# Kernel tuning notes

Hardware: AMD Instinct MI355X
Metric: run time of the kernel (lower is better)

The kernel has to match this reference:

```python
import jax, jax.numpy as jnp
import numpy as np

N = 100000       # num nodes
E = 1000000      # num edges
D_IN = 128       # input feature dim
D_H = 64         # hidden = output dim
EPS = 1e-5       # GraphNorm eps
SLOPE = 0.2      # LeakyReLU negative slope


def _glorot(key, shape):
    lim = float(np.sqrt(6.0 / (shape[0] + shape[1])))
    return jax.random.uniform(key, shape, jnp.float32, -lim, lim)


def setup_inputs() -> dict:
    key = jax.random.key(0)
    ks = jax.random.split(key, 6)
    return {
        "x": jax.random.normal(ks[0], (N, D_IN), jnp.float32),
        "edge_index": jax.random.randint(ks[1], (2, E), 0, N),
        "W_in": _glorot(ks[2], (D_IN, D_H)),
        "b_in": jnp.zeros((D_H,), jnp.float32),
        "W1": _glorot(ks[3], (D_H, D_H)),
        "b1": jnp.zeros((D_H,), jnp.float32),
        "gn1_alpha": jnp.ones((D_H,), jnp.float32),
        "gn1_gamma": jnp.ones((D_H,), jnp.float32),
        "gn1_beta": jnp.zeros((D_H,), jnp.float32),
        "W2": _glorot(ks[4], (D_H, D_H)),
        "b2": jnp.zeros((D_H,), jnp.float32),
        "gn2_alpha": jnp.ones((D_H,), jnp.float32),
        "gn2_gamma": jnp.ones((D_H,), jnp.float32),
        "gn2_beta": jnp.zeros((D_H,), jnp.float32),
    }


def gcn_conv(x, W, b, src, dst):
    # GCNConv with added self-loops and symmetric normalization:
    # out = D^{-1/2} (A + I) D^{-1/2} (x W) + b
    xw = x @ W                                                 # [N, D]
    ones = jnp.ones((src.shape[0],), x.dtype)
    deg = jax.ops.segment_sum(ones, dst, num_segments=x.shape[0]) + 1.0  # +1 self-loop
    dinv = jax.lax.rsqrt(deg)                                  # [N]
    coef = dinv[src] * dinv[dst]                               # [E]
    agg = jax.ops.segment_sum(xw[src] * coef[:, None], dst, num_segments=x.shape[0])
    return agg + xw * (dinv * dinv)[:, None] + b


def graph_norm(x, alpha, gamma, beta):
    # PyG GraphNorm over a single graph: per-feature mean/var over all nodes
    mean = jnp.mean(x, axis=0)
    c = x - alpha * mean
    var = jnp.mean(c * c, axis=0)
    return gamma * c * jax.lax.rsqrt(var + EPS) + beta


def reference(x, edge_index, W_in, b_in, W1, b1, gn1_alpha, gn1_gamma, gn1_beta,
              W2, b2, gn2_alpha, gn2_gamma, gn2_beta):
    src, dst = edge_index[0], edge_index[1]
    h = x @ W_in + b_in                                        # input projection
    h = graph_norm(gcn_conv(h, W1, b1, src, dst), gn1_alpha, gn1_gamma, gn1_beta)
    h = jnp.where(h > 0, h, SLOPE * h)                         # LeakyReLU(0.2); dropout=eval (identity)
    h = graph_norm(gcn_conv(h, W2, b2, src, dst), gn2_alpha, gn2_gamma, gn2_beta)
    return h                                                    # [N, D_H]
```

## Files before the change

kernel.cpp:

```cpp
#include <hip/hip_runtime.h>
#include <stdint.h>

#define N_NODES 100000
#define N_EDGES 1000000
#define D_IN 128
#define D_H 64
#define EPS 1e-5f
#define SLOPE 0.2f

typedef unsigned short u16;
typedef unsigned int u32;
typedef __attribute__((ext_vector_type(8))) short bf16x8;
typedef __attribute__((ext_vector_type(4))) float f32x4;

__device__ __forceinline__ float bf2f(u16 u) {
    union { u32 i; float f; } v; v.i = ((u32)u) << 16; return v.f;
}
__device__ __forceinline__ u16 f2bf(float f) {
    union { float f; u32 i; } v; v.f = f;
    u32 r = (v.i + 0x7fffu + ((v.i >> 16) & 1u)) >> 16;
    return (u16)r;
}
__device__ __forceinline__ bool is_f32(const void* flagp) {
    return *(const u32*)flagp == 0x3F800000u;
}
__device__ __forceinline__ float loadf(const void* p, size_t i, bool m) {
    return m ? ((const float*)p)[i] : bf2f(((const u16*)p)[i]);
}

__global__ void kprep(const void* __restrict__ W_in, const void* __restrict__ b_in,
                      const void* __restrict__ W1, const void* __restrict__ W2,
                      const void* __restrict__ flagp,
                      u16* __restrict__ WcT, u16* __restrict__ W2T,
                      float* __restrict__ bc, u16* __restrict__ xwb_pad)
{
    bool m = is_f32(flagp);
    int t = threadIdx.x;
    if (blockIdx.x < 64) {
        int c = blockIdx.x;
        __shared__ float w1c[D_H];
        if (t < D_H) w1c[t] = loadf(W1, t * D_H + c, m);
        __syncthreads();
        float acc = 0.f;
        #pragma unroll 8
        for (int j = 0; j < D_H; j++) acc += loadf(W_in, t * D_H + j, m) * w1c[j];
        WcT[c * D_IN + t] = f2bf(acc);
        if (t == 0) {
            float b = 0.f;
            for (int j = 0; j < D_H; j++) b += loadf(b_in, j, m) * w1c[j];
            bc[c] = b;
        }
        if (c == 0 && t < D_H) xwb_pad[(size_t)N_NODES * D_H + t] = 0;
    } else {
        int idx = (blockIdx.x - 64) * 128 + t;
        int n = idx >> 6, k = idx & 63;
        W2T[n * D_H + k] = f2bf(loadf(W2, k * D_H + n, m));
    }
}

__global__ void kfill(const int* __restrict__ ei, int* __restrict__ cnt,
                      int* __restrict__ bucket)
{
    int e = blockIdx.x * blockDim.x + threadIdx.x;
    if (e >= N_EDGES) return;
    int s = ei[e];
    int d = ei[N_EDGES + e];
    int slot = atomicAdd(&cnt[d], 1);
    if (slot < 64) bucket[(size_t)d * 64 + slot] = s;
}

__global__ __launch_bounds__(256) void kgemm1(const void* __restrict__ x,
        const u16* __restrict__ WcT, const float* __restrict__ bc,
        const int* __restrict__ cnt, const void* __restrict__ flagp,
        u16* __restrict__ xwb)
{
    bool m = is_f32(flagp);
    __shared__ __align__(16) u16 xs[64 * 136];
    __shared__ __align__(16) u16 WT[64 * 136];
    int tid = threadIdx.x;
    int row0 = blockIdx.x * 64;
    for (int i = tid; i < 64 * 32; i += 256) {
        int r = i >> 5, kq = (i & 31) * 4;
        *(ushort4*)(WT + r * 136 + kq) = *(const ushort4*)(WcT + r * D_IN + kq);
    }
    for (int i = tid; i < 64 * 32; i += 256) {
        int r = i >> 5, kq = (i & 31) * 4;
        int gr = row0 + r;
        ushort4 u = make_ushort4(0, 0, 0, 0);
        if (gr < N_NODES) {
            if (m) {
                float4 v = *(const float4*)((const float*)x + (size_t)gr * D_IN + kq);
                u = make_ushort4(f2bf(v.x), f2bf(v.y), f2bf(v.z), f2bf(v.w));
            } else {
                u = *(const ushort4*)((const u16*)x + (size_t)gr * D_IN + kq);
            }
        }
        *(ushort4*)(xs + r * 136 + kq) = u;
    }
    __syncthreads();
    int w = tid >> 6, L = tid & 63;
    int q = L >> 4, c = L & 15;
    f32x4 acc[4];
    #pragma unroll
    for (int ct = 0; ct < 4; ct++) {
        float b = bc[ct * 16 + c];
        acc[ct] = (f32x4){b, b, b, b};
    }
    const u16* ap = xs + (w * 16 + c) * 136 + q * 8;
    #pragma unroll
    for (int kk = 0; kk < 4; kk++) {
        bf16x8 af = *(const bf16x8*)(ap + kk * 32);
        #pragma unroll
        for (int ct = 0; ct < 4; ct++) {
            bf16x8 bfr = *(const bf16x8*)(WT + (ct * 16 + c) * 136 + kk * 32 + q * 8);
            acc[ct] = __builtin_amdgcn_mfma_f32_16x16x32_bf16(af, bfr, acc[ct], 0, 0, 0);
        }
    }
    #pragma unroll
    for (int r = 0; r < 4; r++) {
        int gr = row0 + w * 16 + q * 4 + r;
        if (gr < N_NODES) {
            float ds = rsqrtf((float)cnt[gr] + 1.0f);
            #pragma unroll
            for (int ct = 0; ct < 4; ct++)
                xwb[(size_t)gr * D_H + ct * 16 + c] = f2bf(acc[ct][r] * ds);
        }
    }
}

__global__ __launch_bounds__(256) void kagg(const u16* __restrict__ xwb,
        const int* __restrict__ cnt, const int* __restrict__ bucket,
        const void* __restrict__ bvec, const void* __restrict__ flagp,
        u16* __restrict__ ybuf, float* __restrict__ accum)
{
    bool m = is_f32(flagp);
    __shared__ __align__(16) char smem[4][8192];
    __shared__ float red_s[4][64], red_q[4][64];
    int tid = threadIdx.x;
    int wv = tid >> 6, L = tid & 63;
    int half = L >> 5, mm = L & 31;
    int node0 = blockIdx.x * 32 + wv * 8;

    int cnt8 = cnt[node0 + (L & 7)];
    int deg[8]; float dd[8];
    #pragma unroll
    for (int t = 0; t < 8; t++) {
        int cv = __builtin_amdgcn_readlane(cnt8, t);
        deg[t] = min(cv, 64);
        dd[t] = rsqrtf((float)cv + 1.0f);
    }
    float b0 = loadf(bvec, 2 * mm, m), b1 = loadf(bvec, 2 * mm + 1, m);

    int tl = L >> 4, sl = L & 15;
    int raw0 = bucket[(size_t)(node0 + tl) * 64 + sl];
    int raw1 = bucket[(size_t)(node0 + 4 + tl) * 64 + sl];

    float ls0 = 0, ls1 = 0, lq0 = 0, lq1 = 0;
    char* base = &smem[wv][0];

    #pragma unroll
    for (int b = 0; b < 2; b++) {
        int nb = node0 + b * 4;
        int raw = b ? raw1 : raw0;
        int i_l = nb + tl;
        int degL = min(__shfl(cnt8, b * 4 + tl), 64);
        int src = (sl < degL) ? raw : ((sl == degL) ? i_l : N_NODES);

        #pragma unroll
        for (int k = 0; k < 8; k++) {
            if ((k & 1) == 0 || deg[b * 4 + (k >> 1)] + 1 > 8) {
                int srcK = __shfl(src, k * 8 + (L >> 3));
                const u16* gp = xwb + (size_t)srcK * D_H + (L & 7) * 8;
                __builtin_amdgcn_global_load_lds(gp, base + k * 1024, 16, 0, 0);
            }
        }
        __builtin_amdgcn_s_waitcnt(0);
        __builtin_amdgcn_sched_barrier(0);
        asm volatile("" ::: "memory");

        float A0 = 0, A1 = 0, C0 = 0, C1 = 0;
        #pragma unroll
        for (int p = 0; p < 2; p++) {
            int np = p * 2 + half;
            const u32* rp = (const u32*)(base + np * 2048);
            int dnp = half ? deg[b * 4 + p * 2 + 1] : deg[b * 4 + p * 2];
            float a0 = 0, a1 = 0;
            #pragma unroll
            for (int s = 0; s < 8; s++) {
                u32 v = rp[s * 32 + mm];
                a0 += __uint_as_float(v << 16);
                a1 += __uint_as_float(v & 0xffff0000u);
            }
            if (dnp + 1 > 8) {
                #pragma unroll
                for (int s = 8; s < 16; s++) {
                    u32 v = rp[s * 32 + mm];
                    a0 += __uint_as_float(v << 16);
                    a1 += __uint_as_float(v & 0xffff0000u);
                }
            }
            if (p == 0) { A0 = a0; A1 = a1; } else { C0 = a0; C1 = a1; }
        }
        #pragma unroll
        for (int t = 0; t < 4; t++) {
            int degt = deg[b * 4 + t];
            if (degt >= 16) {
                int i = nb + t;
                float r0 = 0, r1 = 0;
                for (int s = 16 + half; s <= degt; s += 2) {
                    int sv = (s < degt) ? bucket[(size_t)i * 64 + s] : i;
                    u32 v = *((const u32*)(xwb + (size_t)sv * D_H) + mm);
                    r0 += __uint_as_float(v << 16);
                    r1 += __uint_as_float(v & 0xffff0000u);
                }
                r0 += __shfl_xor(r0, 32);
                r1 += __shfl_xor(r1, 32);
                bool mine = (half == (t & 1));
                if (t < 2) { A0 += mine ? r0 : 0.f; A1 += mine ? r1 : 0.f; }
                else       { C0 += mine ? r0 : 0.f; C1 += mine ? r1 : 0.f; }
            }
        }
        #pragma unroll
        for (int p = 0; p < 2; p++) {
            float a0 = p ? C0 : A0, a1 = p ? C1 : A1;
            float ddv = half ? dd[b * 4 + p * 2 + 1] : dd[b * 4 + p * 2];
            float y0 = ddv * a0 + b0;
            float y1 = ddv * a1 + b1;
            int node = nb + p * 2 + half;
            ((u32*)(ybuf + (size_t)node * D_H))[mm] =
                (u32)f2bf(y0) | ((u32)f2bf(y1) << 16);
            ls0 += y0; ls1 += y1; lq0 += y0 * y0; lq1 += y1 * y1;
        }
        asm volatile("" ::: "memory");
    }

    ls0 += __shfl_xor(ls0, 32); ls1 += __shfl_xor(ls1, 32);
    lq0 += __shfl_xor(lq0, 32); lq1 += __shfl_xor(lq1, 32);
    if (half == 0) {
        *(float2*)&red_s[wv][2 * mm] = make_float2(ls0, ls1);
        *(float2*)&red_q[wv][2 * mm] = make_float2(lq0, lq1);
    }
    __syncthreads();
    if (tid < 64) {
        atomicAdd(&accum[tid],      red_s[0][tid] + red_s[1][tid] + red_s[2][tid] + red_s[3][tid]);
        atomicAdd(&accum[64 + tid], red_q[0][tid] + red_q[1][tid] + red_q[2][tid] + red_q[3][tid]);
    }
}

__global__ __launch_bounds__(256) void kgemm2(const u16* __restrict__ y1b,
        const u16* __restrict__ W2T, const float* __restrict__ accum,
        const void* __restrict__ alpha, const void* __restrict__ gamma,
        const void* __restrict__ beta, const void* __restrict__ flagp,
        const int* __restrict__ cnt, u16* __restrict__ xwb)
{
    bool m = is_f32(flagp);
    __shared__ __align__(16) u16 hs[64 * 72];
    __shared__ __align__(16) u16 WT[64 * 72];
    __shared__ float aL[64], cL[64];
    int tid = threadIdx.x;
    if (tid < 64) {
        float mean = accum[tid] * (1.0f / N_NODES);
        float al = loadf(alpha, tid, m);
        float var = accum[64 + tid] * (1.0f / N_NODES) - mean * mean * al * (2.0f - al);
        var = fmaxf(var, 0.f);
        float a = loadf(gamma, tid, m) * rsqrtf(var + EPS);
        aL[tid] = a;
        cL[tid] = loadf(beta, tid, m) - a * al * mean;
    }
    for (int i = tid; i < 64 * 16; i += 256) {
        int r = i >> 4, kq = (i & 15) * 4;
        *(ushort4*)(WT + r * 72 + kq) = *(const ushort4*)(W2T + r * D_H + kq);
    }
    __syncthreads();
    int row0 = blockIdx.x * 64;
    for (int i = tid; i < 64 * 16; i += 256) {
        int r = i >> 4, kq = (i & 15) * 4;
        int gr = row0 + r;
        ushort4 u = make_ushort4(0, 0, 0, 0);
        if (gr < N_NODES) u = *(const ushort4*)(y1b + (size_t)gr * D_H + kq);
        float h0 = aL[kq + 0] * bf2f(u.x) + cL[kq + 0]; h0 = h0 > 0.f ? h0 : SLOPE * h0;
        float h1 = aL[kq + 1] * bf2f(u.y) + cL[kq + 1]; h1 = h1 > 0.f ? h1 : SLOPE * h1;
        float h2 = aL[kq + 2] * bf2f(u.z) + cL[kq + 2]; h2 = h2 > 0.f ? h2 : SLOPE * h2;
        float h3 = aL[kq + 3] * bf2f(u.w) + cL[kq + 3]; h3 = h3 > 0.f ? h3 : SLOPE * h3;
        *(ushort4*)(hs + r * 72 + kq) = make_ushort4(f2bf(h0), f2bf(h1), f2bf(h2), f2bf(h3));
    }
    __syncthreads();
    int w = tid >> 6, L = tid & 63;
    int q = L >> 4, c = L & 15;
    f32x4 acc[4] = {};
    const u16* ap = hs + (w * 16 + c) * 72 + q * 8;
    #pragma unroll
    for (int kk = 0; kk < 2; kk++) {
        bf16x8 af = *(const bf16x8*)(ap + kk * 32);
        #pragma unroll
        for (int ct = 0; ct < 4; ct++) {
            bf16x8 bfr = *(const bf16x8*)(WT + (ct * 16 + c) * 72 + kk * 32 + q * 8);
            acc[ct] = __builtin_amdgcn_mfma_f32_16x16x32_bf16(af, bfr, acc[ct], 0, 0, 0);
        }
    }
    #pragma unroll
    for (int r = 0; r < 4; r++) {
        int gr = row0 + w * 16 + q * 4 + r;
        if (gr < N_NODES) {
            float ds = rsqrtf((float)cnt[gr] + 1.0f);
            #pragma unroll
            for (int ct = 0; ct < 4; ct++)
                xwb[(size_t)gr * D_H + ct * 16 + c] = f2bf(acc[ct][r] * ds);
        }
    }
}

__global__ __launch_bounds__(256) void kout(const u16* __restrict__ y2b,
        const float* __restrict__ accum2, const void* __restrict__ alpha,
        const void* __restrict__ gamma, const void* __restrict__ beta,
        const void* __restrict__ flagp, void* __restrict__ out)
{
    bool m = is_f32(flagp);
    __shared__ float a2[64], c2[64];
    int tid = threadIdx.x;
    if (tid < 64) {
        float mean = accum2[tid] * (1.0f / N_NODES);
        float al = loadf(alpha, tid, m);
        float var = accum2[64 + tid] * (1.0f / N_NODES) - mean * mean * al * (2.0f - al);
        var = fmaxf(var, 0.f);
        float a = loadf(gamma, tid, m) * rsqrtf(var + EPS);
        a2[tid] = a;
        c2[tid] = loadf(beta, tid, m) - a * al * mean;
    }
    __syncthreads();
    int w0 = (blockIdx.x * 256 + tid) * 2;
    u32 v0 = ((const u32*)y2b)[w0];
    u32 v1 = ((const u32*)y2b)[w0 + 1];
    int f = (w0 * 2) & 63;
    float o0 = a2[f + 0] * __uint_as_float(v0 << 16)          + c2[f + 0];
    float o1 = a2[f + 1] * __uint_as_float(v0 & 0xffff0000u)  + c2[f + 1];
    float o2 = a2[f + 2] * __uint_as_float(v1 << 16)          + c2[f + 2];
    float o3 = a2[f + 3] * __uint_as_float(v1 & 0xffff0000u)  + c2[f + 3];
    if (m) {
        *(float4*)((float*)out + (size_t)w0 * 2) = make_float4(o0, o1, o2, o3);
    } else {
        u32 p0 = (u32)f2bf(o0) | ((u32)f2bf(o1) << 16);
        u32 p1 = (u32)f2bf(o2) | ((u32)f2bf(o3) << 16);
        *(uint2*)((u32*)out + w0) = make_uint2(p0, p1);
    }
}

extern "C" void kernel_launch(void* const* d_in, const int* in_sizes, int n_in,
                              void* d_out, int out_size, void* d_ws, size_t ws_size,
                              hipStream_t stream)
{
    const void* x    = d_in[0];
    const int*  ei   = (const int*)d_in[1];
    const void* W_in = d_in[2];
    const void* b_in = d_in[3];
    const void* W1   = d_in[4];
    const void* b1   = d_in[5];
    const void* gn1a = d_in[6];
    const void* gn1g = d_in[7];
    const void* gn1b = d_in[8];
    const void* W2   = d_in[9];
    const void* b2   = d_in[10];
    const void* gn2a = d_in[11];
    const void* gn2g = d_in[12];
    const void* gn2b = d_in[13];

    char* ws = (char*)d_ws;
    int*   cnt    = (int*)(ws + 0);
    float* accum  = (float*)(ws + 400000);
    float* bc     = (float*)(ws + 402048);
    u16*   WcT    = (u16*)(ws + 402432);
    u16*   W2T    = (u16*)(ws + 418816);
    int*   bucket = (int*)(ws + 1235200);
    u16*   bufA   = (u16*)(ws + 26835200);
    u16*   bufB   = (u16*)(ws + 39635456);

    hipMemsetAsync(ws, 0, 400000 + 1024, stream);

    kprep<<<96, 128, 0, stream>>>(W_in, b_in, W1, W2, gn1a, WcT, W2T, bc, bufA);
    kfill<<<(N_EDGES + 255) / 256, 256, 0, stream>>>(ei, cnt, bucket);
    kgemm1<<<(N_NODES + 63) / 64, 256, 0, stream>>>(x, WcT, bc, cnt, gn1a, bufA);
    kagg<<<N_NODES / 32, 256, 0, stream>>>(bufA, cnt, bucket, b1, gn1a, bufB, accum);
    kgemm2<<<(N_NODES + 63) / 64, 256, 0, stream>>>(bufB, W2T, accum, gn1a, gn1g, gn1b, gn1a, cnt, bufA);
    kagg<<<N_NODES / 32, 256, 0, stream>>>(bufA, cnt, bucket, b2, gn1a, bufB, accum + 128);
    kout<<<N_NODES * D_H / 1024, 256, 0, stream>>>(bufB, accum + 128, gn2a, gn2g, gn2b, gn1a, d_out);
}
```

Baseline: 397.2 us.

## Replace LDS-staged neighbor gather with register double-buffered direct loads in aggregation

The aggregation kernel no longer stages neighbor rows into shared memory with global_load_lds and a full waitcnt barrier. Each half-wave now gathers its node's 16 neighbor slots straight into registers and prefetches the next node's 16 rows while summing the current ones, so loads overlap with compute across four node groups. This removes the LDS round trip and the per-batch stalls, but always issues 16 loads per node, including padded slots that point at the dummy row, and roughly doubles the register footprint for the gather buffers.

```diff
diff --git a/kernel.cpp b/kernel.cpp
--- a/kernel.cpp
+++ b/kernel.cpp
@@ -134,7 +134,6 @@
         u16* __restrict__ ybuf, float* __restrict__ accum)
 {
     bool m = is_f32(flagp);
-    __shared__ __align__(16) char smem[4][8192];
     __shared__ float red_s[4][64], red_q[4][64];
     int tid = threadIdx.x;
     int wv = tid >> 6, L = tid & 63;
@@ -142,96 +141,64 @@
     int node0 = blockIdx.x * 32 + wv * 8;
 
     int cnt8 = cnt[node0 + (L & 7)];
-    int deg[8]; float dd[8];
-    #pragma unroll
-    for (int t = 0; t < 8; t++) {
-        int cv = __builtin_amdgcn_readlane(cnt8, t);
-        deg[t] = min(cv, 64);
-        dd[t] = rsqrtf((float)cv + 1.0f);
-    }
-    float b0 = loadf(bvec, 2 * mm, m), b1 = loadf(bvec, 2 * mm + 1, m);
-
     int tl = L >> 4, sl = L & 15;
     int raw0 = bucket[(size_t)(node0 + tl) * 64 + sl];
     int raw1 = bucket[(size_t)(node0 + 4 + tl) * 64 + sl];
 
+    float b0 = loadf(bvec, 2 * mm, m), b1 = loadf(bvec, 2 * mm + 1, m);
     float ls0 = 0, ls1 = 0, lq0 = 0, lq1 = 0;
-    char* base = &smem[wv][0];
-
-    #pragma unroll
-    for (int b = 0; b < 2; b++) {
-        int nb = node0 + b * 4;
-        int raw = b ? raw1 : raw0;
-        int i_l = nb + tl;
-        int degL = min(__shfl(cnt8, b * 4 + tl), 64);
-        int src = (sl < degL) ? raw : ((sl == degL) ? i_l : N_NODES);
-
+
+    const char* xb = (const char*)xwb;
+    u32 moff = (u32)(mm << 2);
+
+    auto srcof = [&](int g, int s, int degn, int ng) -> u32 {
+        int rw = __shfl((g < 2) ? raw0 : raw1, (((g & 1) * 2 + half) << 4) + s);
+        int sv = (s < degn) ? rw : ((s == degn) ? ng : N_NODES);
+        return ((u32)sv << 7) | moff;
+    };
+
+    int cvg = __shfl(cnt8, half);
+    int degn = min(cvg, 64);
+    int ng = node0 + half;
+    u32 cur[16];
+    #pragma unroll
+    for (int s = 0; s < 16; s++)
+        cur[s] = *(const u32*)(xb + srcof(0, s, degn, ng));
+
+    #pragma unroll
+    for (int g = 0; g < 4; g++) {
+        u32 nxt[16];
+        int cvn = 0, degx = 0, ngx = 0;
+        if (g < 3) {
+            cvn = __shfl(cnt8, 2 * (g + 1) + half);
+            degx = min(cvn, 64);
+            ngx = node0 + 2 * (g + 1) + half;
+            #pragma unroll
+            for (int s = 0; s < 16; s++)
+                nxt[s] = *(const u32*)(xb + srcof(g + 1, s, degx, ngx));
+        }
+        float a0 = 0.f, a1 = 0.f;
         #pragma unroll
-        for (int k = 0; k < 8; k++) {
-            if ((k & 1) == 0 || deg[b * 4 + (k >> 1)] + 1 > 8) {
-                int srcK = __shfl(src, k * 8 + (L >> 3));
-                const u16* gp = xwb + (size_t)srcK * D_H + (L & 7) * 8;
-                __builtin_amdgcn_global_load_lds(gp, base + k * 1024, 16, 0, 0);
-            }
-        }
-        __builtin_amdgcn_s_waitcnt(0);
-        __builtin_amdgcn_sched_barrier(0);
-        asm volatile("" ::: "memory");
-
-        float A0 = 0, A1 = 0, C0 = 0, C1 = 0;
-        #pragma unroll
-        for (int p = 0; p < 2; p++) {
-            int np = p * 2 + half;
-            const u32* rp = (const u32*)(base + np * 2048);
-            int dnp = half ? deg[b * 4 + p * 2 + 1] : deg[b * 4 + p * 2];
-            float a0 = 0, a1 = 0;
-            #pragma unroll
-            for (int s = 0; s < 8; s++) {
-                u32 v = rp[s * 32 + mm];
+        for (int s = 0; s < 16; s++) {
+            a0 += __uint_as_float(cur[s] << 16);
+            a1 += __uint_as_float(cur[s] & 0xffff0000u);
+        }
+        if (degn >= 16) {
+            for (int s = 16; s <= degn; s++) {
+                int sv = (s < degn) ? bucket[(size_t)ng * 64 + s] : ng;
+                u32 v = *(const u32*)(xb + (((u32)sv << 7) | moff));
                 a0 += __uint_as_float(v << 16);
                 a1 += __uint_as_float(v & 0xffff0000u);
             }
-            if (dnp + 1 > 8) {
-                #pragma unroll
-                for (int s = 8; s < 16; s++) {
-                    u32 v = rp[s * 32 + mm];
-                    a0 += __uint_as_float(v << 16);
-                    a1 += __uint_as_float(v & 0xffff0000u);
-                }
-            }
-            if (p == 0) { A0 = a0; A1 = a1; } else { C0 = a0; C1 = a1; }
-        }
+        }
+        float ddn = rsqrtf((float)cvg + 1.0f);
+        float y0 = ddn * a0 + b0;
+        float y1 = ddn * a1 + b1;
+        ((u32*)(ybuf + (size_t)ng * D_H))[mm] = (u32)f2bf(y0) | ((u32)f2bf(y1) << 16);
+        ls0 += y0; ls1 += y1; lq0 += y0 * y0; lq1 += y1 * y1;
         #pragma unroll
-        for (int t = 0; t < 4; t++) {
-            int degt = deg[b * 4 + t];
-            if (degt >= 16) {
-                int i = nb + t;
-                float r0 = 0, r1 = 0;
-                for (int s = 16 + half; s <= degt; s += 2) {
-                    int sv = (s < degt) ? bucket[(size_t)i * 64 + s] : i;
-                    u32 v = *((const u32*)(xwb + (size_t)sv * D_H) + mm);
-                    r0 += __uint_as_float(v << 16);
-                    r1 += __uint_as_float(v & 0xffff0000u);
-                }
-                r0 += __shfl_xor(r0, 32);
-                r1 += __shfl_xor(r1, 32);
-                bool mine = (half == (t & 1));
-                if (t < 2) { A0 += mine ? r0 : 0.f; A1 += mine ? r1 : 0.f; }
-                else       { C0 += mine ? r0 : 0.f; C1 += mine ? r1 : 0.f; }
-            }
-        }
-        #pragma unroll
-        for (int p = 0; p < 2; p++) {
-            float a0 = p ? C0 : A0, a1 = p ? C1 : A1;
-            float ddv = half ? dd[b * 4 + p * 2 + 1] : dd[b * 4 + p * 2];
-            float y0 = ddv * a0 + b0;
-            float y1 = ddv * a1 + b1;
-            int node = nb + p * 2 + half;
-            ((u32*)(ybuf + (size_t)node * D_H))[mm] =
-                (u32)f2bf(y0) | ((u32)f2bf(y1) << 16);
-            ls0 += y0; ls1 += y1; lq0 += y0 * y0; lq1 += y1 * y1;
-        }
-        asm volatile("" ::: "memory");
+        for (int s = 0; s < 16; s++) cur[s] = nxt[s];
+        cvg = cvn; degn = degx; ng = ngx;
     }
 
     ls0 += __shfl_xor(ls0, 32); ls1 += __shfl_xor(ls1, 32);
```

Measured after the change: 392.1 us. About the same (-1.3%).
